# Kernel tuning notes

Hardware: AMD Instinct MI355X
Metric: run time of the kernel (lower is better)

The kernel has to match this reference:

```python
import jax, jax.numpy as jnp
import numpy as np

B, S, P, K, D, H = 16384, 512, 1024, 8, 64, 128


def setup_inputs() -> dict:
    key = jax.random.key(0)
    ks = jax.random.split(key, 8)
    return {
        "skl_pfc": jax.random.normal(ks[0], (B, S), dtype=jnp.float32),
        "tensor_mask": jnp.ones((B, P), dtype=jnp.float32),
        "skl_emd": jax.random.normal(ks[1], (S, D), dtype=jnp.float32),
        "plm_emd": jax.random.normal(ks[2], (P, D), dtype=jnp.float32),
        "W": jax.random.normal(ks[3], (H, D), dtype=jnp.float32) * 0.05,
        "U": jax.random.normal(ks[4], (H, D), dtype=jnp.float32) * 0.05,
        "v_T": jax.random.normal(ks[5], (1, H), dtype=jnp.float32) * 0.05,
        "group_idx": jax.random.randint(ks[6], (P, K), 0, S, dtype=jnp.int64),
    }


def reference(skl_pfc, tensor_mask, skl_emd, plm_emd, W, U, v_T, group_idx):
    # Per problem p: align = v_T @ tanh(W @ plm_p + U @ skl_emd[S_p].T)
    proj_p = plm_emd @ W.T                       # [P, H]
    proj_s = (skl_emd @ U.T)[group_idx]          # [P, K, H] gather of projected skills
    scores = jnp.einsum("h,pkh->pk", v_T[0], jnp.tanh(proj_p[:, None, :] + proj_s))  # [P, K]
    att = jax.nn.softmax(scores, axis=-1)        # softmax over each problem's skill group
    # Weighted sum of gathered skill proficiencies -> per-problem proficiency
    out = jnp.einsum("bpk,pk->bp", skl_pfc[:, group_idx], att)  # [B, P]
    return out * tensor_mask
```

## Files before the change

### kernel.cpp

```cpp
#include <hip/hip_runtime.h>
#include <cmath>

#define B_ 16384
#define S_ 512
#define P_ 1024
#define K_ 8
#define D_ 64
#define H_ 128
#define BT 16

__global__ __launch_bounds__(128) void proj_skl_kernel(
    const float* __restrict__ skl_emd, const float* __restrict__ U,
    float* __restrict__ sklproj) {
  __shared__ float row[D_];
  const int s = blockIdx.x, h = threadIdx.x;
  if (h < D_) row[h] = skl_emd[s * D_ + h];
  __syncthreads();
  float acc = 0.f;
#pragma unroll
  for (int d = 0; d < D_; d++) acc += row[d] * U[h * D_ + d];
  sklproj[s * H_ + h] = acc;
}

__global__ __launch_bounds__(128) void att_kernel(
    const float* __restrict__ plm_emd, const float* __restrict__ W,
    const float* __restrict__ vT, const float* __restrict__ sklproj,
    const int* __restrict__ gidx, float* __restrict__ att) {
  __shared__ float prow[D_];
  __shared__ float red[2][K_];
  const int p = blockIdx.x, h = threadIdx.x;
  if (h < D_) prow[h] = plm_emd[p * D_ + h];
  __syncthreads();
  float pp = 0.f;
#pragma unroll
  for (int d = 0; d < D_; d++) pp += prow[d] * W[h * D_ + d];
  const float v = vT[h];
  int g[K_];
#pragma unroll
  for (int k = 0; k < K_; k++) g[k] = gidx[p * K_ + k];
  float partial[K_];
#pragma unroll
  for (int k = 0; k < K_; k++) partial[k] = v * tanhf(pp + sklproj[g[k] * H_ + h]);
#pragma unroll
  for (int off = 32; off >= 1; off >>= 1)
#pragma unroll
    for (int k = 0; k < K_; k++) partial[k] += __shfl_down(partial[k], off, 64);
  const int wave = h >> 6, lane = h & 63;
  if (lane == 0)
#pragma unroll
    for (int k = 0; k < K_; k++) red[wave][k] = partial[k];
  __syncthreads();
  if (h == 0) {
    float s[K_], m = -1e30f;
#pragma unroll
    for (int k = 0; k < K_; k++) { s[k] = red[0][k] + red[1][k]; m = fmaxf(m, s[k]); }
    float denom = 0.f;
#pragma unroll
    for (int k = 0; k < K_; k++) { s[k] = expf(s[k] - m); denom += s[k]; }
    const float inv = 1.f / denom;
#pragma unroll
    for (int k = 0; k < K_; k++) att[p * K_ + k] = s[k] * inv;
  }
}

__global__ __launch_bounds__(256) void out_kernel(
    const float* __restrict__ skl_pfc, const float* __restrict__ mask,
    const float* __restrict__ att, const int* __restrict__ gidx,
    float* __restrict__ out) {
  __shared__ float rows[BT][S_];
  const int t = threadIdx.x;
  const int b0 = blockIdx.x * BT;

  const float4* __restrict__ src = (const float4*)(skl_pfc + (size_t)b0 * S_);
  float4* dst = (float4*)(&rows[0][0]);
#pragma unroll
  for (int i = 0; i < (BT * S_ / 4) / 256; i++) dst[t + i * 256] = src[t + i * 256];

  float a[4][K_];
  int g[4][K_];
#pragma unroll
  for (int j = 0; j < 4; j++) {
    const int p = t + j * 256;
    const float4* ap = (const float4*)(att + p * K_);
    const int4* gp = (const int4*)(gidx + p * K_);
    float4 a0 = ap[0], a1 = ap[1];
    int4 g0 = gp[0], g1 = gp[1];
    a[j][0] = a0.x; a[j][1] = a0.y; a[j][2] = a0.z; a[j][3] = a0.w;
    a[j][4] = a1.x; a[j][5] = a1.y; a[j][6] = a1.z; a[j][7] = a1.w;
    g[j][0] = g0.x; g[j][1] = g0.y; g[j][2] = g0.z; g[j][3] = g0.w;
    g[j][4] = g1.x; g[j][5] = g1.y; g[j][6] = g1.z; g[j][7] = g1.w;
  }
  __syncthreads();

  for (int bb = 0; bb < BT; bb++) {
    const size_t rowoff = (size_t)(b0 + bb) * P_;
    const float* __restrict__ r = rows[bb];
#pragma unroll
    for (int j = 0; j < 4; j++) {
      const int p = t + j * 256;
      float acc = 0.f;
#pragma unroll
      for (int k = 0; k < K_; k++) acc += r[g[j][k]] * a[j][k];
      out[rowoff + p] = acc * mask[rowoff + p];
    }
  }
}

extern "C" void kernel_launch(void* const* d_in, const int* in_sizes, int n_in,
                              void* d_out, int out_size, void* d_ws, size_t ws_size,
                              hipStream_t stream) {
  const float* skl_pfc = (const float*)d_in[0];
  const float* mask    = (const float*)d_in[1];
  const float* skl_emd = (const float*)d_in[2];
  const float* plm_emd = (const float*)d_in[3];
  const float* W       = (const float*)d_in[4];
  const float* U       = (const float*)d_in[5];
  const float* vT      = (const float*)d_in[6];
  const int*   gidx    = (const int*)d_in[7];
  float* out = (float*)d_out;

  float* sklproj = (float*)d_ws;
  float* att     = sklproj + S_ * H_;

  proj_skl_kernel<<<S_, 128, 0, stream>>>(skl_emd, U, sklproj);
  att_kernel<<<P_, 128, 0, stream>>>(plm_emd, W, vT, sklproj, gidx, att);
  out_kernel<<<B_ / BT, 256, 0, stream>>>(skl_pfc, mask, att, gidx, out);
}
```

Measured before the change: 185.7 us.

## Transpose skill rows in LDS so each gather reads eight batches vectorized

The output kernel now stores the skl_pfc tile transposed as [S][PAD] in shared memory. Each gathered skill index then yields eight batch values through two float4 LDS reads, instead of one scalar read per batch row. The batch tile drops from 16 to 8, with a min-blocks occupancy hint of 6, so LDS use shrinks and more blocks fit per CU. The per-problem att and gidx loads now happen inside the loop rather than being held in registers across batches. The price is a strided, non-vectorized global load during the transpose and twice as many blocks re-reading att and gidx.

Result: faster. 177.5 us (-4.4%).

```diff
diff --git a/kernel.cpp b/kernel.cpp
--- a/kernel.cpp
+++ b/kernel.cpp
@@ -7,7 +7,8 @@
 #define K_ 8
 #define D_ 64
 #define H_ 128
-#define BT 16
+#define BT 8
+#define PAD 12
 
 __global__ __launch_bounds__(128) void proj_skl_kernel(
     const float* __restrict__ skl_emd, const float* __restrict__ U,
@@ -63,45 +64,48 @@
   }
 }
 
-__global__ __launch_bounds__(256) void out_kernel(
+__global__ __launch_bounds__(256, 6) void out_kernel(
     const float* __restrict__ skl_pfc, const float* __restrict__ mask,
     const float* __restrict__ att, const int* __restrict__ gidx,
     float* __restrict__ out) {
-  __shared__ float rows[BT][S_];
+  __shared__ __align__(16) float rows_T[S_][PAD];
   const int t = threadIdx.x;
   const int b0 = blockIdx.x * BT;
 
-  const float4* __restrict__ src = (const float4*)(skl_pfc + (size_t)b0 * S_);
-  float4* dst = (float4*)(&rows[0][0]);
 #pragma unroll
-  for (int i = 0; i < (BT * S_ / 4) / 256; i++) dst[t + i * 256] = src[t + i * 256];
+  for (int i = 0; i < S_ / 256; i++) {
+    const int s = t + i * 256;
+    float vals[BT];
+#pragma unroll
+    for (int bb = 0; bb < BT; bb++) vals[bb] = skl_pfc[(size_t)(b0 + bb) * S_ + s];
+    float4* wp = (float4*)&rows_T[s][0];
+    wp[0] = make_float4(vals[0], vals[1], vals[2], vals[3]);
+    wp[1] = make_float4(vals[4], vals[5], vals[6], vals[7]);
+  }
+  __syncthreads();
 
-  float a[4][K_];
-  int g[4][K_];
-#pragma unroll
   for (int j = 0; j < 4; j++) {
     const int p = t + j * 256;
     const float4* ap = (const float4*)(att + p * K_);
     const int4* gp = (const int4*)(gidx + p * K_);
-    float4 a0 = ap[0], a1 = ap[1];
-    int4 g0 = gp[0], g1 = gp[1];
-    a[j][0] = a0.x; a[j][1] = a0.y; a[j][2] = a0.z; a[j][3] = a0.w;
-    a[j][4] = a1.x; a[j][5] = a1.y; a[j][6] = a1.z; a[j][7] = a1.w;
-    g[j][0] = g0.x; g[j][1] = g0.y; g[j][2] = g0.z; g[j][3] = g0.w;
-    g[j][4] = g1.x; g[j][5] = g1.y; g[j][6] = g1.z; g[j][7] = g1.w;
-  }
-  __syncthreads();
-
-  for (int bb = 0; bb < BT; bb++) {
-    const size_t rowoff = (size_t)(b0 + bb) * P_;
-    const float* __restrict__ r = rows[bb];
+    const float4 a0 = ap[0], a1 = ap[1];
+    const int4 g0 = gp[0], g1 = gp[1];
+    const float av[K_] = {a0.x, a0.y, a0.z, a0.w, a1.x, a1.y, a1.z, a1.w};
+    const int gv[K_] = {g0.x, g0.y, g0.z, g0.w, g1.x, g1.y, g1.z, g1.w};
+    float acc[BT] = {0.f, 0.f, 0.f, 0.f, 0.f, 0.f, 0.f, 0.f};
 #pragma unroll
-    for (int j = 0; j < 4; j++) {
-      const int p = t + j * 256;
-      float acc = 0.f;
+    for (int k = 0; k < K_; k++) {
+      const float4* rp = (const float4*)&rows_T[gv[k]][0];
+      const float4 v0 = rp[0];
+      const float4 v1 = rp[1];
+      const float a = av[k];
+      acc[0] += v0.x * a; acc[1] += v0.y * a; acc[2] += v0.z * a; acc[3] += v0.w * a;
+      acc[4] += v1.x * a; acc[5] += v1.y * a; acc[6] += v1.z * a; acc[7] += v1.w * a;
+    }
 #pragma unroll
-      for (int k = 0; k < K_; k++) acc += r[g[j][k]] * a[j][k];
-      out[rowoff + p] = acc * mask[rowoff + p];
+    for (int bb = 0; bb < BT; bb++) {
+      const size_t off = (size_t)(b0 + bb) * P_ + p;
+      out[off] = acc[bb] * mask[off];
     }
   }
 }
```
